# Kernel tuning notes

Measured on AMD Instinct MI355X. Metric: run time of the kernel, lower is better.

The kernel has to match this reference:

```python
import jax, jax.numpy as jnp
import numpy as np

SEGMENT_LENGTHS = [1024, 4096]
DILATION_RATES = [1, 2]
HILBERT_CHUNK = 4096
B, N, H, D = 2, 4096, 16, 64


def _hilbert_mapping(n: int) -> np.ndarray:
    """Replicates _generate_hilbert_curve: gather indices for a length-n chunk."""
    if n <= 64:
        return np.arange(n, dtype=np.int64)
    size = 1
    while size * size < n:
        size *= 2

    def d2xy(nn, d):
        x = y = 0
        s = 1
        while s < nn:
            rx = 1 if (d // 2) & 1 else 0
            ry = 1 if (d ^ rx) & 1 else 0
            if ry == 0:
                if rx == 1:
                    x, y = nn - 1 - x, nn - 1 - y
                x, y = y, x
            x += s * rx
            y += s * ry
            d //= 4
            s *= 2
        return x, y

    mapping = np.zeros(n, dtype=np.int64)
    h2l = {}
    for i in range(min(n, size * size)):
        x, y = d2xy(size, i)
        li = y * size + x
        if li < n:
            h2l[i] = li
    hidx = 0
    for i in sorted(h2l):
        mapping[h2l[i]] = hidx
        hidx += 1
    return mapping


def _apply_hilbert(t: jnp.ndarray) -> jnp.ndarray:
    # t: [b, n, h, d]; reorder sequence within HILBERT_CHUNK-sized chunks.
    n = t.shape[1]
    chunks = []
    for start in range(0, n, HILBERT_CHUNK):
        end = min(start + HILBERT_CHUNK, n)
        m = jnp.asarray(_hilbert_mapping(end - start))
        chunks.append(t[:, start:end][:, m])
    return jnp.concatenate(chunks, axis=1) if len(chunks) > 1 else chunks[0]


def _dilation_indices(s: int, r: int, offset: int) -> np.ndarray:
    # Replicates _create_dilation_pattern
    idx = np.arange(offset, s, r, dtype=np.int64)
    expected = (s + r - 1 - offset) // r
    if idx.shape[0] > expected:
        idx = idx[:expected]
    elif idx.shape[0] < expected:
        pad = np.arange(expected - idx.shape[0], dtype=np.int64) % idx.shape[0]
        idx = np.concatenate([idx, idx[pad]])
    return idx


def _dilated_attention(q, k, v):
    # LongNet-style dilated attention: heads partitioned across groups;
    # each group attends within segments over dilated positions.
    b, n, h, d = q.shape
    G = len(SEGMENT_LENGTHS)
    hg = h // G
    scale = 1.0 / np.sqrt(d).astype(np.float32)
    out = jnp.zeros_like(q)
    for g, (s, r) in enumerate(zip(SEGMENT_LENGTHS, DILATION_RATES)):
        offset = g % r
        idx = jnp.asarray(_dilation_indices(s, r, offset))
        hs = slice(g * hg, (g + 1) * hg)
        # [b, n//s, s, hg, d] -> dilated [b, n//s, s/r, hg, d]
        qg = q[:, :, hs].reshape(b, n // s, s, hg, d)[:, :, idx]
        kg = k[:, :, hs].reshape(b, n // s, s, hg, d)[:, :, idx]
        vg = v[:, :, hs].reshape(b, n // s, s, hg, d)[:, :, idx]
        att = jnp.einsum('bgqhd,bgkhd->bghqk', qg, kg) * scale
        att = jax.nn.softmax(att, axis=-1)
        og = jnp.einsum('bghqk,bgkhd->bgqhd', att, vg)
        full = jnp.zeros((b, n // s, s, hg, d), q.dtype).at[:, :, idx].set(og)
        out = out.at[:, :, hs].set(full.reshape(b, n, hg, d))
    return out


def setup_inputs() -> dict:
    key = jax.random.key(0)
    kq, kk, kv = jax.random.split(key, 3)
    q = jax.random.normal(kq, (B, N, H, D), dtype=jnp.float32)
    k = jax.random.normal(kk, (B, N, H, D), dtype=jnp.float32)
    v = jax.random.normal(kv, (B, N, H, D), dtype=jnp.float32)
    return {'q': q, 'k': k, 'v': v}


def reference(q, k, v):
    k_h = _apply_hilbert(k)
    v_h = _apply_hilbert(v)
    return _dilated_attention(q, k_h, v_h)
```

## Files before the change

kernel.cpp:

```cpp
#include <hip/hip_runtime.h>
#include <hip/hip_bf16.h>

#define N_ 4096
#define H_ 16
#define D_ 64
#define G1ROWOFF 65536

typedef __attribute__((ext_vector_type(4))) float f32x4;
typedef __attribute__((ext_vector_type(8))) _Float16 f16x8;

#define AS1 __attribute__((address_space(1)))
#define AS3 __attribute__((address_space(3)))

__device__ __forceinline__ unsigned int pkrtz(float a, float b){
  auto h = __builtin_amdgcn_cvt_pkrtz(a, b);
  unsigned int r; __builtin_memcpy(&r, &h, 4); return r;
}
__device__ __forceinline__ unsigned int pku(unsigned int lo, unsigned int hi){
  return lo | (hi << 16);
}

__global__ __launch_bounds__(1024) void hilbert_map_kernel(int* __restrict__ mapping){
  __shared__ int sm[4096];
  const int t = threadIdx.x;
#pragma unroll
  for(int jj=0;jj<4;jj++) mapping[t*4+jj] = 0;
  int li_a[4], val_a[4];
#pragma unroll
  for(int jj=0;jj<4;jj++){
    int i = t*4+jj;
    int x=0,y=0,d=i;
#pragma unroll
    for(int s=1;s<64;s<<=1){
      int rx=(d>>1)&1;
      int ry=(d^rx)&1;
      if(ry==0){
        if(rx==1){ x=63-x; y=63-y; }
        int tp=x; x=y; y=tp;
      }
      x+=s*rx; y+=s*ry;
      d>>=2;
    }
    int li=y*64+x;
    li_a[jj]=li;
    val_a[jj]=(li<4096)?1:0;
    sm[i]=val_a[jj];
  }
  __syncthreads();
  for(int off=1;off<4096;off<<=1){
    int v[4];
#pragma unroll
    for(int jj=0;jj<4;jj++){
      int i=t*4+jj;
      v[jj]=sm[i]+((i>=off)?sm[i-off]:0);
    }
    __syncthreads();
#pragma unroll
    for(int jj=0;jj<4;jj++) sm[t*4+jj]=v[jj];
    __syncthreads();
  }
#pragma unroll
  for(int jj=0;jj<4;jj++){
    if(val_a[jj]){
      int rank=sm[t*4+jj]-1;
      int li=li_a[jj];
      int wi=(li>=0)?li:(4096+li);
      if(wi>=0 && wi<4096) atomicMax(&mapping[wi], rank);
    }
  }
}

__global__ __launch_bounds__(256) void prep_kv_kernel(
    const float* __restrict__ K, const float* __restrict__ V,
    const int* __restrict__ hmap,
    unsigned short* __restrict__ Kh, unsigned short* __restrict__ Vt)
{
  __shared__ unsigned short Vlds[64*72];
  const int bid = blockIdx.x, tid = threadIdx.x;
  int b, h, dstRowBase, srcRow;
  const int r = tid>>2, part = tid&3;
  if (bid < 1024){
    int t64 = bid&63; h = (bid>>6)&7; b = bid>>9;
    dstRowBase = (b*8+h)*4096 + t64*64;
    srcRow = t64*64 + r;
  } else {
    int bid2 = bid-1024;
    int t64 = bid2&31; int h8 = (bid2>>5)&7; b = bid2>>8; h = 8+h8;
    dstRowBase = G1ROWOFF + (b*8+h8)*2048 + t64*64;
    srcRow = 1 + 2*(t64*64 + r);
  }
  const int src = hmap[srcRow];
  const size_t sb = (((size_t)(b*N_+src))*H_ + h)*D_ + part*16;
  {
    const float4* kp = (const float4*)(K + sb);
    float4 a=kp[0], c=kp[1], e=kp[2], g=kp[3];
    uint4 w0, w1;
    w0.x=pkrtz(a.x,a.y); w0.y=pkrtz(a.z,a.w); w0.z=pkrtz(c.x,c.y); w0.w=pkrtz(c.z,c.w);
    w1.x=pkrtz(e.x,e.y); w1.y=pkrtz(e.z,e.w); w1.z=pkrtz(g.x,g.y); w1.w=pkrtz(g.z,g.w);
    char* dst = (char*)Kh + ((size_t)(dstRowBase+r))*128;
    *(uint4*)(dst + ((2*part  )^(r&7))*16) = w0;
    *(uint4*)(dst + ((2*part+1)^(r&7))*16) = w1;
  }
  {
    const float4* vp = (const float4*)(V + sb);
    float4 a=vp[0], c=vp[1], e=vp[2], g=vp[3];
    uint4 w0, w1;
    w0.x=pkrtz(a.x,a.y); w0.y=pkrtz(a.z,a.w); w0.z=pkrtz(c.x,c.y); w0.w=pkrtz(c.z,c.w);
    w1.x=pkrtz(e.x,e.y); w1.y=pkrtz(e.z,e.w); w1.z=pkrtz(g.x,g.y); w1.w=pkrtz(g.z,g.w);
    uint4* dst=(uint4*)&Vlds[r*72 + part*16];
    dst[0]=w0; dst[1]=w1;
  }
  __syncthreads();
  {
    const int d = tid>>2, p2 = tid&3;
    unsigned int w0[4], w1[4];
#pragma unroll
    for(int c=0;c<2;c++){
      int kb = 32*c + 4*p2;
      unsigned int* w = c ? w1 : w0;
      w[0] = pku(Vlds[(kb+ 0)*72+d], Vlds[(kb+ 1)*72+d]);
      w[1] = pku(Vlds[(kb+ 2)*72+d], Vlds[(kb+ 3)*72+d]);
      w[2] = pku(Vlds[(kb+16)*72+d], Vlds[(kb+17)*72+d]);
      w[3] = pku(Vlds[(kb+18)*72+d], Vlds[(kb+19)*72+d]);
    }
    char* dst = (char*)Vt + ((size_t)(dstRowBase+d))*128;
    *(uint4*)(dst + ((p2  )^(d&7))*16) = *(uint4*)w0;
    *(uint4*)(dst + ((p2+4)^(d&7))*16) = *(uint4*)w1;
  }
}

__global__ __launch_bounds__(256, 2) void dilated_attn_kernel(
    const float* __restrict__ Q, const unsigned short* __restrict__ Kh,
    const unsigned short* __restrict__ Vt, float* __restrict__ Out)
{
  __shared__ __align__(16) char smem[32768];

  const int bid = blockIdx.x, tid = threadIdx.x;
  const int wave = tid>>6, lane = tid&63;
  const int lr = lane&15, lg = lane>>4;

  int b, outH, qstep, qoff, njobs, nrj;
  int qloc[2];
  size_t kb0, kb1;
  if (bid < 256){
    int xcd = bid&7, idx = bid>>3;
    int kblk = idx&15, Hp = idx>>4;
    int H = xcd + 8*Hp;
    b = H>>3; outH = 8 + (H&7);
    qstep = 2; qoff = 1; njobs = 1; nrj = 16;
    qloc[0] = kblk*128; qloc[1] = qloc[0];
    size_t rowBase = (size_t)G1ROWOFF + (size_t)H*2048;
    kb0 = rowBase*128; kb1 = kb0 + 16*8192;
    int i = tid>>1, half = tid&1;
    int zpos = 2*(qloc[0] + i);
    float4 z = {0.f,0.f,0.f,0.f};
    float4* op = (float4*)(Out + (((size_t)(b*N_+zpos))*H_ + outH)*D_ + half*32);
#pragma unroll
    for(int j=0;j<8;j++) op[j]=z;
  } else {
    int p = bid - 256;
    int xcd = p&7, idx = p>>3;
    int pair = idx&3, Gp = idx>>2;
    int G = xcd + 8*Gp;
    b = G>>5; int seg=(G>>3)&3; int h=G&7; outH=h;
    qstep = 1; qoff = 0; njobs = 2; nrj = 8;
    qloc[0] = seg*1024 + pair*128;
    qloc[1] = seg*1024 + (pair+4)*128;
    size_t rowBase = ((size_t)(b*8+h))*4096 + (size_t)seg*1024;
    kb0 = rowBase*128; kb1 = kb0;
  }

  const float SCL = 0.125f * 1.4426950408889634f;
  f16x8 qf[2][2];
  f32x4 acc[2][4];
  f32x4 accl[2];
  const f32x4 FZ = {0.f,0.f,0.f,0.f};
  union{ unsigned int u[4]; f16x8 v; } ONES;
  ONES.u[0]=0x3C003C00u; ONES.u[1]=0x3C003C00u; ONES.u[2]=0x3C003C00u; ONES.u[3]=0x3C003C00u;

  auto loadQ = [&](int ql0){
#pragma unroll
    for(int qs=0;qs<2;qs++){
      int qpos = qoff + qstep*(ql0 + wave*32 + qs*16 + lr);
      const float* qp = Q + (((size_t)(b*N_+qpos))*H_ + outH)*D_;
#pragma unroll
      for(int dc=0;dc<2;dc++){
        float4 a = *(const float4*)(qp + dc*32 + lg*8);
        float4 c = *(const float4*)(qp + dc*32 + lg*8 + 4);
        union{ unsigned int u[4]; f16x8 v; } pk;
        pk.u[0]=pkrtz(a.x*SCL,a.y*SCL); pk.u[1]=pkrtz(a.z*SCL,a.w*SCL);
        pk.u[2]=pkrtz(c.x*SCL,c.y*SCL); pk.u[3]=pkrtz(c.z*SCL,c.w*SCL);
        qf[qs][dc]=pk.v;
      }
    }
  };

  const int swz = lr&7;
  const int kA0 = lr*128 + ((  lg)^swz)*16;
  const int kA1 = lr*128 + ((4+lg)^swz)*16;
  const int vG0 = lr*128 + ((  lg)^swz)*16;
  const int vG1 = lr*128 + ((4+lg)^swz)*16;

  const int stW = wave*2048 + lane*16;
  auto stageK = [&](int bufOff, int t){
    size_t off = ((t>=16)? kb1 : kb0) + (size_t)(t&15)*8192 + stW;
    const char* gsrc = (const char*)Kh + off;
    char* ldst = smem + bufOff + stW;
#pragma unroll
    for(int i=0;i<2;i++){
      __builtin_amdgcn_global_load_lds((const AS1 void*)(gsrc + i*1024),
                                       (AS3 void*)(ldst + i*1024), 16, 0, 0);
    }
  };

  auto epilogue = [&](int ql0){
#pragma unroll
    for(int qs=0;qs<2;qs++)
#pragma unroll
      for(int r=0;r<4;r++){
        float inv = 1.0f/accl[qs][r];
        int qpos = qoff + qstep*(ql0 + wave*32 + qs*16 + lg*4 + r);
        float* op = Out + (((size_t)(b*N_+qpos))*H_ + outH)*D_ + lr;
#pragma unroll
        for(int dt=0;dt<4;dt++) op[dt*16] = acc[qs][dt][r]*inv;
      }
  };

  stageK(0, 0); stageK(8192, 1);
  int p = 0;
  for(int j=0; j<njobs; ++j){
    loadQ(qloc[j]);
#pragma unroll
    for(int qs=0;qs<2;qs++){
#pragma unroll
      for(int dt=0;dt<4;dt++) acc[qs][dt] = FZ;
      accl[qs] = FZ;
    }
    for(int r=0; r<nrj; ++r, ++p){
      asm volatile("s_waitcnt vmcnt(0)" ::: "memory");
      __builtin_amdgcn_s_barrier();
      const int half = (p&1)*16384;
      if (p < 15){
        const int oth = ((p+1)&1)*16384;
        stageK(oth, 2*p+2); stageK(oth+8192, 2*p+3);
      }
      const char* smA = smem + half;
      const char* smB = smem + half + 8192;

      const int tA = 2*p, tB = 2*p+1;
      const char* gVA = (const char*)Vt + ((tA>=16)? kb1 : kb0) + (size_t)(tA&15)*8192;
      const char* gVB = (const char*)Vt + ((tB>=16)? kb1 : kb0) + (size_t)(tB&15)*8192;
      uint4 vfA[2][4], vfB[2][4];
#pragma unroll
      for(int c=0;c<2;c++){
        const int vGc = c ? vG1 : vG0;
#pragma unroll
        for(int dt=0;dt<4;dt++){
          vfA[c][dt] = *(const uint4*)(gVA + vGc + dt*2048);
          vfB[c][dt] = *(const uint4*)(gVB + vGc + dt*2048);
        }
      }

      f32x4 sA[2][4], sB[2][4];
#pragma unroll
      for(int kt=0;kt<4;kt++){
        f16x8 k0 = *(const f16x8*)(smA + kA0 + kt*2048);
        f16x8 k1 = *(const f16x8*)(smA + kA1 + kt*2048);
#pragma unroll
        for(int qs=0;qs<2;qs++){
          sA[qs][kt] = __builtin_amdgcn_mfma_f32_16x16x32_f16(k0, qf[qs][0], FZ, 0,0,0);
          sA[qs][kt] = __builtin_amdgcn_mfma_f32_16x16x32_f16(k1, qf[qs][1], sA[qs][kt],0,0,0);
        }
      }

      unsigned int UA[2][4][2], UB[2][4][2];
#pragma unroll
      for(int kt=0;kt<4;kt++){
        f16x8 k0 = *(const f16x8*)(smB + kA0 + kt*2048);
        f16x8 k1 = *(const f16x8*)(smB + kA1 + kt*2048);
        sB[0][kt] = __builtin_amdgcn_mfma_f32_16x16x32_f16(k0, qf[0][0], FZ, 0,0,0);
        UA[0][kt][0] = pkrtz(__builtin_amdgcn_exp2f(sA[0][kt][0]),
                             __builtin_amdgcn_exp2f(sA[0][kt][1]));
        sB[0][kt] = __builtin_amdgcn_mfma_f32_16x16x32_f16(k1, qf[0][1], sB[0][kt],0,0,0);
        UA[0][kt][1] = pkrtz(__builtin_amdgcn_exp2f(sA[0][kt][2]),
                             __builtin_amdgcn_exp2f(sA[0][kt][3]));
        sB[1][kt] = __builtin_amdgcn_mfma_f32_16x16x32_f16(k0, qf[1][0], FZ, 0,0,0);
        UA[1][kt][0] = pkrtz(__builtin_amdgcn_exp2f(sA[1][kt][0]),
                             __builtin_amdgcn_exp2f(sA[1][kt][1]));
        sB[1][kt] = __builtin_amdgcn_mfma_f32_16x16x32_f16(k1, qf[1][1], sB[1][kt],0,0,0);
        UA[1][kt][1] = pkrtz(__builtin_amdgcn_exp2f(sA[1][kt][2]),
                             __builtin_amdgcn_exp2f(sA[1][kt][3]));
      }
      union{ unsigned int u[4]; f16x8 v; } pfA[2][2];
#pragma unroll
      for(int qs=0;qs<2;qs++)
#pragma unroll
        for(int c=0;c<2;c++){
          pfA[qs][c].u[0]=UA[qs][2*c][0]; pfA[qs][c].u[1]=UA[qs][2*c][1];
          pfA[qs][c].u[2]=UA[qs][2*c+1][0]; pfA[qs][c].u[3]=UA[qs][2*c+1][1];
        }

#pragma unroll
      for(int c=0;c<2;c++){
#pragma unroll
        for(int dt=0;dt<4;dt++){
          f16x8 vf; __builtin_memcpy(&vf, &vfA[c][dt], 16);
          const int bqs = dt>>1, bkt = 2*c + (dt&1);
          acc[0][dt] = __builtin_amdgcn_mfma_f32_16x16x32_f16(pfA[0][c].v, vf, acc[0][dt],0,0,0);
          UB[bqs][bkt][0] = pkrtz(__builtin_amdgcn_exp2f(sB[bqs][bkt][0]),
                                  __builtin_amdgcn_exp2f(sB[bqs][bkt][1]));
          acc[1][dt] = __builtin_amdgcn_mfma_f32_16x16x32_f16(pfA[1][c].v, vf, acc[1][dt],0,0,0);
          UB[bqs][bkt][1] = pkrtz(__builtin_amdgcn_exp2f(sB[bqs][bkt][2]),
                                  __builtin_amdgcn_exp2f(sB[bqs][bkt][3]));
        }
        accl[0] = __builtin_amdgcn_mfma_f32_16x16x32_f16(pfA[0][c].v, ONES.v, accl[0],0,0,0);
        accl[1] = __builtin_amdgcn_mfma_f32_16x16x32_f16(pfA[1][c].v, ONES.v, accl[1],0,0,0);
      }

#pragma unroll
      for(int c=0;c<2;c++){
        union{ unsigned int u[4]; f16x8 v; } pf0, pf1;
        pf0.u[0]=UB[0][2*c][0]; pf0.u[1]=UB[0][2*c][1]; pf0.u[2]=UB[0][2*c+1][0]; pf0.u[3]=UB[0][2*c+1][1];
        pf1.u[0]=UB[1][2*c][0]; pf1.u[1]=UB[1][2*c][1]; pf1.u[2]=UB[1][2*c+1][0]; pf1.u[3]=UB[1][2*c+1][1];
#pragma unroll
        for(int dt=0;dt<4;dt++){
          f16x8 vf; __builtin_memcpy(&vf, &vfB[c][dt], 16);
          acc[0][dt] = __builtin_amdgcn_mfma_f32_16x16x32_f16(pf0.v, vf, acc[0][dt],0,0,0);
          acc[1][dt] = __builtin_amdgcn_mfma_f32_16x16x32_f16(pf1.v, vf, acc[1][dt],0,0,0);
        }
        accl[0] = __builtin_amdgcn_mfma_f32_16x16x32_f16(pf0.v, ONES.v, accl[0],0,0,0);
        accl[1] = __builtin_amdgcn_mfma_f32_16x16x32_f16(pf1.v, ONES.v, accl[1],0,0,0);
      }
    }
    epilogue(qloc[j]);
  }
}

extern "C" void kernel_launch(void* const* d_in, const int* in_sizes, int n_in,
                              void* d_out, int out_size, void* d_ws, size_t ws_size,
                              hipStream_t stream){
  const float* Q = (const float*)d_in[0];
  const float* K = (const float*)d_in[1];
  const float* V = (const float*)d_in[2];
  float* Out = (float*)d_out;

  int* hmap = (int*)d_ws;
  unsigned short* Kh = (unsigned short*)((char*)d_ws + 16384);
  unsigned short* Vt = (unsigned short*)((char*)d_ws + 16384 + 12582912);

  hipLaunchKernelGGL(hilbert_map_kernel, dim3(1), dim3(1024), 0, stream, hmap);
  hipLaunchKernelGGL(prep_kv_kernel, dim3(1536), dim3(256), 0, stream, K, V, hmap, Kh, Vt);
  hipLaunchKernelGGL(dilated_attn_kernel, dim3(512), dim3(256), 0, stream, Q, Kh, Vt, Out);
}
```

Baseline: 70.84 us.

## Shrink attention tiles to 64 queries per block and triple grid size

Each block now handles 64 queries (16 per wave) instead of 128 or two 128-query jobs. Key tiles are staged one at a time in a 16KB double buffer instead of pairs in 32KB. The grid grows from 512 to 1536 blocks and launch bounds rise to 5 blocks per CU, trading K/V reuse per block for higher occupancy and more parallelism. The interleaved two-tile software pipeline of exp and MFMA is dropped, so each wave has less independent work to hide latency, and K/V global traffic roughly doubles.

Result: slower. 86.94 us (+22.7%).

```diff
diff --git a/kernel.cpp b/kernel.cpp
--- a/kernel.cpp
+++ b/kernel.cpp
@@ -129,71 +129,66 @@
   }
 }
 
-__global__ __launch_bounds__(256, 2) void dilated_attn_kernel(
+__global__ __launch_bounds__(256, 5) void dilated_attn_kernel(
     const float* __restrict__ Q, const unsigned short* __restrict__ Kh,
     const unsigned short* __restrict__ Vt, float* __restrict__ Out)
 {
-  __shared__ __align__(16) char smem[32768];
+  __shared__ __align__(16) char smem[16384];
 
   const int bid = blockIdx.x, tid = threadIdx.x;
   const int wave = tid>>6, lane = tid&63;
   const int lr = lane&15, lg = lane>>4;
 
-  int b, outH, qstep, qoff, njobs, nrj;
-  int qloc[2];
-  size_t kb0, kb1;
-  if (bid < 256){
+  int b, outH, qstep, qoff, nt, qloc;
+  size_t kbase;
+  if (bid < 512){
     int xcd = bid&7, idx = bid>>3;
-    int kblk = idx&15, Hp = idx>>4;
+    int kblk = idx&31, Hp = idx>>5;
     int H = xcd + 8*Hp;
     b = H>>3; outH = 8 + (H&7);
-    qstep = 2; qoff = 1; njobs = 1; nrj = 16;
-    qloc[0] = kblk*128; qloc[1] = qloc[0];
-    size_t rowBase = (size_t)G1ROWOFF + (size_t)H*2048;
-    kb0 = rowBase*128; kb1 = kb0 + 16*8192;
-    int i = tid>>1, half = tid&1;
-    int zpos = 2*(qloc[0] + i);
+    qstep = 2; qoff = 1; nt = 32;
+    qloc = kblk*64;
+    kbase = ((size_t)G1ROWOFF + (size_t)H*2048)*128;
+    int i = tid>>2, part = tid&3;
+    int zpos = 2*(qloc + i);
     float4 z = {0.f,0.f,0.f,0.f};
-    float4* op = (float4*)(Out + (((size_t)(b*N_+zpos))*H_ + outH)*D_ + half*32);
-#pragma unroll
-    for(int j=0;j<8;j++) op[j]=z;
+    float4* op = (float4*)(Out + (((size_t)(b*N_+zpos))*H_ + outH)*D_ + part*16);
+    op[0]=z; op[1]=z; op[2]=z; op[3]=z;
   } else {
-    int p = bid - 256;
+    int p = bid - 512;
     int xcd = p&7, idx = p>>3;
-    int pair = idx&3, Gp = idx>>2;
+    int qb = idx&15, Gp = idx>>4;
     int G = xcd + 8*Gp;
     b = G>>5; int seg=(G>>3)&3; int h=G&7; outH=h;
-    qstep = 1; qoff = 0; njobs = 2; nrj = 8;
-    qloc[0] = seg*1024 + pair*128;
-    qloc[1] = seg*1024 + (pair+4)*128;
-    size_t rowBase = ((size_t)(b*8+h))*4096 + (size_t)seg*1024;
-    kb0 = rowBase*128; kb1 = kb0;
+    qstep = 1; qoff = 0; nt = 16;
+    qloc = seg*1024 + qb*64;
+    kbase = (((size_t)(b*8+h))*4096 + (size_t)seg*1024)*128;
   }
 
   const float SCL = 0.125f * 1.4426950408889634f;
-  f16x8 qf[2][2];
-  f32x4 acc[2][4];
-  f32x4 accl[2];
+  f16x8 qf[2];
+  {
+    int qpos = qoff + qstep*(qloc + wave*16 + lr);
+    const float* qp = Q + (((size_t)(b*N_+qpos))*H_ + outH)*D_;
+#pragma unroll
+    for(int dc=0;dc<2;dc++){
+      float4 a = *(const float4*)(qp + dc*32 + lg*8);
+      float4 c = *(const float4*)(qp + dc*32 + lg*8 + 4);
+      union{ unsigned int u[4]; f16x8 v; } pk;
+      pk.u[0]=pkrtz(a.x*SCL,a.y*SCL); pk.u[1]=pkrtz(a.z*SCL,a.w*SCL);
+      pk.u[2]=pkrtz(c.x*SCL,c.y*SCL); pk.u[3]=pkrtz(c.z*SCL,c.w*SCL);
+      qf[dc]=pk.v;
+    }
+  }
+
+  f32x4 acc[4];
+  f32x4 accl;
   const f32x4 FZ = {0.f,0.f,0.f,0.f};
+#pragma unroll
+  for(int dt=0;dt<4;dt++) acc[dt] = FZ;
+  accl = FZ;
   union{ unsigned int u[4]; f16x8 v; } ONES;
   ONES.u[0]=0x3C003C00u; ONES.u[1]=0x3C003C00u; ONES.u[2]=0x3C003C00u; ONES.u[3]=0x3C003C00u;
-
-  auto loadQ = [&](int ql0){
-#pragma unroll
-    for(int qs=0;qs<2;qs++){
-      int qpos = qoff + qstep*(ql0 + wave*32 + qs*16 + lr);
-      const float* qp = Q + (((size_t)(b*N_+qpos))*H_ + outH)*D_;
-#pragma unroll
-      for(int dc=0;dc<2;dc++){
-        float4 a = *(const float4*)(qp + dc*32 + lg*8);
-        float4 c = *(const float4*)(qp + dc*32 + lg*8 + 4);
-        union{ unsigned int u[4]; f16x8 v; } pk;
-        pk.u[0]=pkrtz(a.x*SCL,a.y*SCL); pk.u[1]=pkrtz(a.z*SCL,a.w*SCL);
-        pk.u[2]=pkrtz(c.x*SCL,c.y*SCL); pk.u[3]=pkrtz(c.z*SCL,c.w*SCL);
-        qf[qs][dc]=pk.v;
-      }
-    }
-  };
 
   const int swz = lr&7;
   const int kA0 = lr*128 + ((  lg)^swz)*16;
@@ -203,136 +198,62 @@
 
   const int stW = wave*2048 + lane*16;
   auto stageK = [&](int bufOff, int t){
-    size_t off = ((t>=16)? kb1 : kb0) + (size_t)(t&15)*8192 + stW;
-    const char* gsrc = (const char*)Kh + off;
+    const char* gsrc = (const char*)Kh + kbase + (size_t)t*8192 + stW;
     char* ldst = smem + bufOff + stW;
-#pragma unroll
-    for(int i=0;i<2;i++){
-      __builtin_amdgcn_global_load_lds((const AS1 void*)(gsrc + i*1024),
-                                       (AS3 void*)(ldst + i*1024), 16, 0, 0);
-    }
+    __builtin_amdgcn_global_load_lds((const AS1 void*)(gsrc       ),
+                                     (AS3 void*)(ldst       ), 16, 0, 0);
+    __builtin_amdgcn_global_load_lds((const AS1 void*)(gsrc + 1024),
+                                     (AS3 void*)(ldst + 1024), 16, 0, 0);
   };
 
-  auto epilogue = [&](int ql0){
-#pragma unroll
-    for(int qs=0;qs<2;qs++)
-#pragma unroll
-      for(int r=0;r<4;r++){
-        float inv = 1.0f/accl[qs][r];
-        int qpos = qoff + qstep*(ql0 + wave*32 + qs*16 + lg*4 + r);
-        float* op = Out + (((size_t)(b*N_+qpos))*H_ + outH)*D_ + lr;
-#pragma unroll
-        for(int dt=0;dt<4;dt++) op[dt*16] = acc[qs][dt][r]*inv;
+  stageK(0, 0);
+  for(int t=0; t<nt; ++t){
+    asm volatile("s_waitcnt vmcnt(0)" ::: "memory");
+    __builtin_amdgcn_s_barrier();
+    const int half = (t&1)*8192;
+    if (t+1 < nt) stageK(((t+1)&1)*8192, t+1);
+
+    const char* gV = (const char*)Vt + kbase + (size_t)t*8192;
+    uint4 vf[2][4];
+#pragma unroll
+    for(int c=0;c<2;c++){
+      const int vGc = c ? vG1 : vG0;
+#pragma unroll
+      for(int dt=0;dt<4;dt++) vf[c][dt] = *(const uint4*)(gV + vGc + dt*2048);
+    }
+
+    const char* sm = smem + half;
+    unsigned int U[4][2];
+#pragma unroll
+    for(int kt=0;kt<4;kt++){
+      f16x8 k0 = *(const f16x8*)(sm + kA0 + kt*2048);
+      f16x8 k1 = *(const f16x8*)(sm + kA1 + kt*2048);
+      f32x4 s = __builtin_amdgcn_mfma_f32_16x16x32_f16(k0, qf[0], FZ, 0,0,0);
+      s = __builtin_amdgcn_mfma_f32_16x16x32_f16(k1, qf[1], s, 0,0,0);
+      U[kt][0] = pkrtz(__builtin_amdgcn_exp2f(s[0]), __builtin_amdgcn_exp2f(s[1]));
+      U[kt][1] = pkrtz(__builtin_amdgcn_exp2f(s[2]), __builtin_amdgcn_exp2f(s[3]));
+    }
+
+#pragma unroll
+    for(int c=0;c<2;c++){
+      union{ unsigned int u[4]; f16x8 v; } pf;
+      pf.u[0]=U[2*c][0]; pf.u[1]=U[2*c][1]; pf.u[2]=U[2*c+1][0]; pf.u[3]=U[2*c+1][1];
+#pragma unroll
+      for(int dt=0;dt<4;dt++){
+        f16x8 vfr; __builtin_memcpy(&vfr, &vf[c][dt], 16);
+        acc[dt] = __builtin_amdgcn_mfma_f32_16x16x32_f16(pf.v, vfr, acc[dt], 0,0,0);
       }
-  };
-
-  stageK(0, 0); stageK(8192, 1);
-  int p = 0;
-  for(int j=0; j<njobs; ++j){
-    loadQ(qloc[j]);
-#pragma unroll
-    for(int qs=0;qs<2;qs++){
-#pragma unroll
-      for(int dt=0;dt<4;dt++) acc[qs][dt] = FZ;
-      accl[qs] = FZ;
-    }
-    for(int r=0; r<nrj; ++r, ++p){
-      asm volatile("s_waitcnt vmcnt(0)" ::: "memory");
-      __builtin_amdgcn_s_barrier();
-      const int half = (p&1)*16384;
-      if (p < 15){
-        const int oth = ((p+1)&1)*16384;
-        stageK(oth, 2*p+2); stageK(oth+8192, 2*p+3);
-      }
-      const char* smA = smem + half;
-      const char* smB = smem + half + 8192;
-
-      const int tA = 2*p, tB = 2*p+1;
-      const char* gVA = (const char*)Vt + ((tA>=16)? kb1 : kb0) + (size_t)(tA&15)*8192;
-      const char* gVB = (const char*)Vt + ((tB>=16)? kb1 : kb0) + (size_t)(tB&15)*8192;
-      uint4 vfA[2][4], vfB[2][4];
-#pragma unroll
-      for(int c=0;c<2;c++){
-        const int vGc = c ? vG1 : vG0;
-#pragma unroll
-        for(int dt=0;dt<4;dt++){
-          vfA[c][dt] = *(const uint4*)(gVA + vGc + dt*2048);
-          vfB[c][dt] = *(const uint4*)(gVB + vGc + dt*2048);
-        }
-      }
-
-      f32x4 sA[2][4], sB[2][4];
-#pragma unroll
-      for(int kt=0;kt<4;kt++){
-        f16x8 k0 = *(const f16x8*)(smA + kA0 + kt*2048);
-        f16x8 k1 = *(const f16x8*)(smA + kA1 + kt*2048);
-#pragma unroll
-        for(int qs=0;qs<2;qs++){
-          sA[qs][kt] = __builtin_amdgcn_mfma_f32_16x16x32_f16(k0, qf[qs][0], FZ, 0,0,0);
-          sA[qs][kt] = __builtin_amdgcn_mfma_f32_16x16x32_f16(k1, qf[qs][1], sA[qs][kt],0,0,0);
-        }
-      }
-
-      unsigned int UA[2][4][2], UB[2][4][2];
-#pragma unroll
-      for(int kt=0;kt<4;kt++){
-        f16x8 k0 = *(const f16x8*)(smB + kA0 + kt*2048);
-        f16x8 k1 = *(const f16x8*)(smB + kA1 + kt*2048);
-        sB[0][kt] = __builtin_amdgcn_mfma_f32_16x16x32_f16(k0, qf[0][0], FZ, 0,0,0);
-        UA[0][kt][0] = pkrtz(__builtin_amdgcn_exp2f(sA[0][kt][0]),
-                             __builtin_amdgcn_exp2f(sA[0][kt][1]));
-        sB[0][kt] = __builtin_amdgcn_mfma_f32_16x16x32_f16(k1, qf[0][1], sB[0][kt],0,0,0);
-        UA[0][kt][1] = pkrtz(__builtin_amdgcn_exp2f(sA[0][kt][2]),
-                             __builtin_amdgcn_exp2f(sA[0][kt][3]));
-        sB[1][kt] = __builtin_amdgcn_mfma_f32_16x16x32_f16(k0, qf[1][0], FZ, 0,0,0);
-        UA[1][kt][0] = pkrtz(__builtin_amdgcn_exp2f(sA[1][kt][0]),
-                             __builtin_amdgcn_exp2f(sA[1][kt][1]));
-        sB[1][kt] = __builtin_amdgcn_mfma_f32_16x16x32_f16(k1, qf[1][1], sB[1][kt],0,0,0);
-        UA[1][kt][1] = pkrtz(__builtin_amdgcn_exp2f(sA[1][kt][2]),
-                             __builtin_amdgcn_exp2f(sA[1][kt][3]));
-      }
-      union{ unsigned int u[4]; f16x8 v; } pfA[2][2];
-#pragma unroll
-      for(int qs=0;qs<2;qs++)
-#pragma unroll
-        for(int c=0;c<2;c++){
-          pfA[qs][c].u[0]=UA[qs][2*c][0]; pfA[qs][c].u[1]=UA[qs][2*c][1];
-          pfA[qs][c].u[2]=UA[qs][2*c+1][0]; pfA[qs][c].u[3]=UA[qs][2*c+1][1];
-        }
-
-#pragma unroll
-      for(int c=0;c<2;c++){
-#pragma unroll
-        for(int dt=0;dt<4;dt++){
-          f16x8 vf; __builtin_memcpy(&vf, &vfA[c][dt], 16);
-          const int bqs = dt>>1, bkt = 2*c + (dt&1);
-          acc[0][dt] = __builtin_amdgcn_mfma_f32_16x16x32_f16(pfA[0][c].v, vf, acc[0][dt],0,0,0);
-          UB[bqs][bkt][0] = pkrtz(__builtin_amdgcn_exp2f(sB[bqs][bkt][0]),
-                                  __builtin_amdgcn_exp2f(sB[bqs][bkt][1]));
-          acc[1][dt] = __builtin_amdgcn_mfma_f32_16x16x32_f16(pfA[1][c].v, vf, acc[1][dt],0,0,0);
-          UB[bqs][bkt][1] = pkrtz(__builtin_amdgcn_exp2f(sB[bqs][bkt][2]),
-                                  __builtin_amdgcn_exp2f(sB[bqs][bkt][3]));
-        }
-        accl[0] = __builtin_amdgcn_mfma_f32_16x16x32_f16(pfA[0][c].v, ONES.v, accl[0],0,0,0);
-        accl[1] = __builtin_amdgcn_mfma_f32_16x16x32_f16(pfA[1][c].v, ONES.v, accl[1],0,0,0);
-      }
-
-#pragma unroll
-      for(int c=0;c<2;c++){
-        union{ unsigned int u[4]; f16x8 v; } pf0, pf1;
-        pf0.u[0]=UB[0][2*c][0]; pf0.u[1]=UB[0][2*c][1]; pf0.u[2]=UB[0][2*c+1][0]; pf0.u[3]=UB[0][2*c+1][1];
-        pf1.u[0]=UB[1][2*c][0]; pf1.u[1]=UB[1][2*c][1]; pf1.u[2]=UB[1][2*c+1][0]; pf1.u[3]=UB[1][2*c+1][1];
-#pragma unroll
-        for(int dt=0;dt<4;dt++){
-          f16x8 vf; __builtin_memcpy(&vf, &vfB[c][dt], 16);
-          acc[0][dt] = __builtin_amdgcn_mfma_f32_16x16x32_f16(pf0.v, vf, acc[0][dt],0,0,0);
-          acc[1][dt] = __builtin_amdgcn_mfma_f32_16x16x32_f16(pf1.v, vf, acc[1][dt],0,0,0);
-        }
-        accl[0] = __builtin_amdgcn_mfma_f32_16x16x32_f16(pf0.v, ONES.v, accl[0],0,0,0);
-        accl[1] = __builtin_amdgcn_mfma_f32_16x16x32_f16(pf1.v, ONES.v, accl[1],0,0,0);
-      }
-    }
-    epilogue(qloc[j]);
+      accl = __builtin_amdgcn_mfma_f32_16x16x32_f16(pf.v, ONES.v, accl, 0,0,0);
+    }
+  }
+
+#pragma unroll
+  for(int r=0;r<4;r++){
+    float inv = 1.0f/accl[r];
+    int qpos = qoff + qstep*(qloc + wave*16 + lg*4 + r);
+    float* op = Out + (((size_t)(b*N_+qpos))*H_ + outH)*D_ + lr;
+#pragma unroll
+    for(int dt=0;dt<4;dt++) op[dt*16] = acc[dt][r]*inv;
   }
 }
 
@@ -350,5 +271,5 @@
 
   hipLaunchKernelGGL(hilbert_map_kernel, dim3(1), dim3(1024), 0, stream, hmap);
   hipLaunchKernelGGL(prep_kv_kernel, dim3(1536), dim3(256), 0, stream, K, V, hmap, Kh, Vt);
-  hipLaunchKernelGGL(dilated_attn_kernel, dim3(512), dim3(256), 0, stream, Q, Kh, Vt, Out);
-}
+  hipLaunchKernelGGL(dilated_attn_kernel, dim3(1536), dim3(256), 0, stream, Q, Kh, Vt, Out);
+}
```
